# Kernel optimization log

Hardware: AMD Instinct MI355X
Metric: run time of the kernel (lower is better)

## Reference

```python
import jax, jax.numpy as jnp
import numpy as np

B, T, C, H = 8, 2048, 1024, 64

def setup_inputs() -> dict:
    key = jax.random.key(0)
    k1, k2, k3, k4 = jax.random.split(key, 4)
    x = jax.random.normal(k1, (B, T, C), dtype=jnp.float32)
    # torch nn.Linear default init ~ U(-1/sqrt(in), 1/sqrt(in)); scale kept small for stability
    s = 1.0 / np.sqrt(C)
    Wq = jax.random.uniform(k2, (C, H), dtype=jnp.float32, minval=-s, maxval=s)
    Wk = jax.random.uniform(k3, (C, H), dtype=jnp.float32, minval=-s, maxval=s)
    Wv = jax.random.uniform(k4, (C, H), dtype=jnp.float32, minval=-s, maxval=s)
    return {"x": x, "Wq": Wq, "Wk": Wk, "Wv": Wv}

def reference(x, Wq, Wk, Wv):
    # x: [B,T,C]; Wq/Wk/Wv: [C,H] (equivalent to torch Linear weight transposed)
    Q = jnp.einsum('btc,ch->bth', x, Wq)
    K = jnp.einsum('btc,ch->bth', x, Wk)
    V = jnp.einsum('btc,ch->bth', x, Wv)
    H_ = Q.shape[-1]
    scale = 1.0 / jnp.sqrt(jnp.asarray(H_, dtype=Q.dtype))
    w = jnp.einsum('bqh,bkh->bqk', Q, K) * scale  # [B,T,T]
    T_ = x.shape[1]
    causal = jnp.tril(jnp.ones((T_, T_), dtype=bool))
    w = jnp.where(causal, w, -jnp.inf)
    w = jax.nn.softmax(w, axis=-1)
    out = jnp.einsum('bqk,bkh->bqh', w, V)  # [B,T,H]
    return out
```

## Files before the change

### kernel.cpp

```cpp
#include <hip/hip_runtime.h>
#include <math.h>

#define Bb 8
#define Tt 2048
#define Cc 1024
#define Hh 64
#define BT (Bb * Tt)
#define SLOG2E 0.18033688011112042f

typedef __attribute__((ext_vector_type(8))) short short8;
typedef __attribute__((ext_vector_type(4))) float floatx4;

__device__ inline unsigned short f2bf(float f) {
  unsigned int u = __builtin_bit_cast(unsigned int, f);
  u += 0x7fff + ((u >> 16) & 1);
  return (unsigned short)(u >> 16);
}
__device__ inline float bf2f(unsigned short u) {
  unsigned int x = ((unsigned int)u) << 16;
  return __builtin_bit_cast(float, x);
}

__global__ __launch_bounds__(256) void wconv2(
    const float* __restrict__ Wq, const float* __restrict__ Wk,
    const float* __restrict__ Wv, unsigned short* __restrict__ WTf) {
  int bid = blockIdx.x;
  int w = bid >> 5;
  int kc = bid & 31;
  const float* __restrict__ W = (w == 0) ? Wq : (w == 1 ? Wk : Wv);
  int t = threadIdx.x;
  int hg = t >> 6, quad = (t >> 4) & 3, lrow = t & 15;
  int g = w * 4 + hg;
  int h = hg * 16 + lrow;
  unsigned short tmp[8];
#pragma unroll
  for (int j = 0; j < 8; ++j)
    tmp[j] = f2bf(W[(size_t)(kc * 32 + quad * 8 + j) * Hh + h]);
  unsigned short* dst = &WTf[((size_t)(g * 32 + kc) * 64 + quad * 16 + lrow) * 8];
  *(ushort4*)dst = make_ushort4(tmp[0], tmp[1], tmp[2], tmp[3]);
  *(ushort4*)(dst + 4) = make_ushort4(tmp[4], tmp[5], tmp[6], tmp[7]);
}

__global__ __launch_bounds__(256) void qkv5(
    const float* __restrict__ x, const unsigned short* __restrict__ WTf,
    unsigned short* __restrict__ Qb, unsigned short* __restrict__ Kb,
    unsigned short* __restrict__ VTt) {
  __shared__ __align__(16) unsigned short Af[2048];

  int mt = blockIdx.x;
  int t = threadIdx.x;
  int wv = t >> 6, lane = t & 63;
  int lrow = lane & 15, quad = lane >> 4;

  floatx4 acc[2][3];
#pragma unroll
  for (int g2 = 0; g2 < 2; ++g2)
#pragma unroll
    for (int j = 0; j < 3; ++j)
#pragma unroll
      for (int r = 0; r < 4; ++r) acc[g2][j][r] = 0.f;

  int srow = t >> 3, scg = t & 7;
  int skc2 = scg >> 2, squad = scg & 3;
  int sslot = ((srow >> 4) * 2 + skc2) * 64 + squad * 16 +
              (((srow & 15) + squad + 4 * skc2) & 15);
  const float* xp = x + (size_t)(mt * 32 + srow) * Cc + scg * 8;

  int aslot[2][2];
#pragma unroll
  for (int g2 = 0; g2 < 2; ++g2)
#pragma unroll
    for (int kc2 = 0; kc2 < 2; ++kc2)
      aslot[g2][kc2] = ((g2 * 2 + kc2) * 64 + quad * 16 +
                        ((lrow + quad + 4 * kc2) & 15)) * 8;

  const unsigned short* wbase[3];
#pragma unroll
  for (int j = 0; j < 3; ++j)
    wbase[j] = WTf + (size_t)(wv * 3 + j) * 32 * 512 + lane * 8;

  float4 nv0 = *(const float4*)xp;
  float4 nv1 = *(const float4*)(xp + 4);

  for (int kk = 0; kk < 16; ++kk) {
    __syncthreads();
    short8 a;
    a[0] = (short)f2bf(nv0.x); a[1] = (short)f2bf(nv0.y);
    a[2] = (short)f2bf(nv0.z); a[3] = (short)f2bf(nv0.w);
    a[4] = (short)f2bf(nv1.x); a[5] = (short)f2bf(nv1.y);
    a[6] = (short)f2bf(nv1.z); a[7] = (short)f2bf(nv1.w);
    *(short8*)&Af[sslot * 8] = a;
    if (kk < 15) {
      nv0 = *(const float4*)(xp + (kk + 1) * 64);
      nv1 = *(const float4*)(xp + (kk + 1) * 64 + 4);
    }
    __syncthreads();

    short8 bf[3][2];
    int kg = kk * 2;
#pragma unroll
    for (int j = 0; j < 3; ++j)
#pragma unroll
      for (int kc2 = 0; kc2 < 2; ++kc2)
        bf[j][kc2] = *(const short8*)(wbase[j] + (size_t)(kg + kc2) * 512);
    short8 af[2][2];
#pragma unroll
    for (int g2 = 0; g2 < 2; ++g2)
#pragma unroll
      for (int kc2 = 0; kc2 < 2; ++kc2)
        af[g2][kc2] = *(const short8*)&Af[aslot[g2][kc2]];
#pragma unroll
    for (int g2 = 0; g2 < 2; ++g2)
#pragma unroll
      for (int j = 0; j < 3; ++j) {
        acc[g2][j] = __builtin_amdgcn_mfma_f32_16x16x32_bf16(af[g2][0], bf[j][0], acc[g2][j], 0, 0, 0);
        acc[g2][j] = __builtin_amdgcn_mfma_f32_16x16x32_bf16(af[g2][1], bf[j][1], acc[g2][j], 0, 0, 0);
      }
  }

#pragma unroll
  for (int g2 = 0; g2 < 2; ++g2) {
    int tok0 = mt * 32 + g2 * 16 + quad * 4;
#pragma unroll
    for (int j = 0; j < 3; ++j) {
      int nbase = (wv * 3 + j) * 16;
      if (nbase >= 128) {
        int h = nbase - 128 + lrow;
        *(ushort4*)&VTt[(size_t)(tok0 >> 6) * 4096 + h * 64 + (tok0 & 63)] =
            make_ushort4(f2bf(acc[g2][j][0]), f2bf(acc[g2][j][1]),
                         f2bf(acc[g2][j][2]), f2bf(acc[g2][j][3]));
      } else {
        unsigned short* dst = (nbase >= 64) ? Kb : Qb;
        int col = (nbase & 63) + lrow;
#pragma unroll
        for (int r = 0; r < 4; ++r)
          dst[(size_t)(tok0 + r) * Hh + col] = f2bf(acc[g2][j][r]);
      }
    }
  }
}

__global__ __launch_bounds__(512) void attn3(
    const unsigned short* __restrict__ Qb, const unsigned short* __restrict__ Kb,
    const unsigned short* __restrict__ VTt, float* __restrict__ out) {
  __shared__ __align__(16) unsigned char smem[33 * 1024];
  unsigned short* Pall = (unsigned short*)smem;
  unsigned short* Ocomb = (unsigned short*)smem;
  float* Lcomb = (float*)(smem + 32768);

  int bid = blockIdx.x;
  int b = bid >> 5;
  int j = bid & 31;
  int t = threadIdx.x;
  int wv = t >> 6, lane = t & 63;
  int lrow = lane & 15, quad = lane >> 4;

  unsigned short* Pw = Pall + wv * 2048;

  short8 ones;
#pragma unroll
  for (int i = 0; i < 8; ++i) ones[i] = (short)0x3F80;

  for (int half = 0; half < 2; ++half) {
    int qt = half ? (63 - j) : j;
    int q0 = qt * 32;
    int nkt = (qt >> 1) + 1;

    short8 aq[2][2];
#pragma unroll
    for (int qs = 0; qs < 2; ++qs)
#pragma unroll
      for (int kc = 0; kc < 2; ++kc)
        aq[qs][kc] = *(const short8*)
            &Qb[(size_t)(b * Tt + q0 + qs * 16 + lrow) * Hh + kc * 32 + quad * 8];

    floatx4 acc_o[2][4];
    floatx4 acc_l[2];
#pragma unroll
    for (int qs = 0; qs < 2; ++qs) {
#pragma unroll
      for (int r = 0; r < 4; ++r) acc_l[qs][r] = 0.f;
#pragma unroll
      for (int hs = 0; hs < 4; ++hs)
#pragma unroll
        for (int r = 0; r < 4; ++r) acc_o[qs][hs][r] = 0.f;
    }

    for (int kt = wv; kt < nkt; kt += 8) {
      int kbase = b * Tt + kt * 64;
      short8 kf[4][2], vf[4][2];
#pragma unroll
      for (int sn = 0; sn < 4; ++sn)
#pragma unroll
        for (int kc = 0; kc < 2; ++kc)
          kf[sn][kc] = *(const short8*)
              &Kb[(size_t)(kbase + sn * 16 + lrow) * Hh + kc * 32 + quad * 8];
      int ktile = b * 32 + kt;
#pragma unroll
      for (int hs = 0; hs < 4; ++hs)
#pragma unroll
        for (int kc = 0; kc < 2; ++kc)
          vf[hs][kc] = *(const short8*)
              &VTt[(size_t)ktile * 4096 + (hs * 16 + lrow) * 64 + kc * 32 + quad * 8];

      floatx4 s[2][4];
#pragma unroll
      for (int qs = 0; qs < 2; ++qs)
#pragma unroll
        for (int sn = 0; sn < 4; ++sn) {
          floatx4 z;
#pragma unroll
          for (int r = 0; r < 4; ++r) z[r] = 0.f;
          z = __builtin_amdgcn_mfma_f32_16x16x32_bf16(aq[qs][0], kf[sn][0], z, 0, 0, 0);
          z = __builtin_amdgcn_mfma_f32_16x16x32_bf16(aq[qs][1], kf[sn][1], z, 0, 0, 0);
          s[qs][sn] = z;
        }

      bool diag = (kt == nkt - 1);
#pragma unroll
      for (int qs = 0; qs < 2; ++qs)
#pragma unroll
        for (int sn = 0; sn < 4; ++sn) {
          int k5 = (sn & 1) * 16 + lrow;
          int slot = qs * 2 + (sn >> 1);
          int rlbase = (k5 >> 3) * 16;
#pragma unroll
          for (int r = 0; r < 4; ++r) {
            float v = s[qs][sn][r] * SLOG2E;
            if (diag) {
              int gk = kt * 64 + sn * 16 + lrow;
              int gq = q0 + qs * 16 + quad * 4 + r;
              if (gk > gq) v = -INFINITY;
            }
            float p = exp2f(v);
            Pw[slot * 512 + (rlbase + quad * 4 + r) * 8 + (k5 & 7)] = f2bf(p);
          }
        }

      short8 ap[2][2];
#pragma unroll
      for (int qs = 0; qs < 2; ++qs)
#pragma unroll
        for (int kc = 0; kc < 2; ++kc)
          ap[qs][kc] = *(const short8*)&Pw[(qs * 2 + kc) * 512 + lane * 8];

#pragma unroll
      for (int qs = 0; qs < 2; ++qs) {
        acc_l[qs] = __builtin_amdgcn_mfma_f32_16x16x32_bf16(ap[qs][0], ones, acc_l[qs], 0, 0, 0);
        acc_l[qs] = __builtin_amdgcn_mfma_f32_16x16x32_bf16(ap[qs][1], ones, acc_l[qs], 0, 0, 0);
#pragma unroll
        for (int hs = 0; hs < 4; ++hs) {
          acc_o[qs][hs] = __builtin_amdgcn_mfma_f32_16x16x32_bf16(ap[qs][0], vf[hs][0], acc_o[qs][hs], 0, 0, 0);
          acc_o[qs][hs] = __builtin_amdgcn_mfma_f32_16x16x32_bf16(ap[qs][1], vf[hs][1], acc_o[qs][hs], 0, 0, 0);
        }
      }
    }

#pragma unroll
    for (int qs = 0; qs < 2; ++qs)
#pragma unroll
      for (int hs = 0; hs < 4; ++hs) {
        int s8 = qs * 4 + hs;
        *(ushort4*)&Ocomb[((wv * 8 + s8) * 64 + lane) * 4] =
            make_ushort4(f2bf(acc_o[qs][hs][0]), f2bf(acc_o[qs][hs][1]),
                         f2bf(acc_o[qs][hs][2]), f2bf(acc_o[qs][hs][3]));
      }
    if (lrow == 0) {
#pragma unroll
      for (int qs = 0; qs < 2; ++qs)
#pragma unroll
        for (int r = 0; r < 4; ++r)
          Lcomb[wv * 32 + qs * 16 + quad * 4 + r] = acc_l[qs][r];
    }
    __syncthreads();

    {
      int qsub = wv >> 2, hs = wv & 3;
      float o[4] = {0.f, 0.f, 0.f, 0.f};
#pragma unroll
      for (int w = 0; w < 8; ++w) {
        ushort4 pk = *(const ushort4*)&Ocomb[((w * 8 + wv) * 64 + lane) * 4];
        o[0] += bf2f(pk.x); o[1] += bf2f(pk.y);
        o[2] += bf2f(pk.z); o[3] += bf2f(pk.w);
      }
#pragma unroll
      for (int r = 0; r < 4; ++r) {
        float lv = 0.f;
#pragma unroll
        for (int w = 0; w < 8; ++w)
          lv += Lcomb[w * 32 + qsub * 16 + quad * 4 + r];
        int row = q0 + qsub * 16 + quad * 4 + r;
        out[(size_t)(b * Tt + row) * Hh + hs * 16 + lrow] = o[r] / lv;
      }
    }
    __syncthreads();
  }
}

extern "C" void kernel_launch(void* const* d_in, const int* in_sizes, int n_in,
                              void* d_out, int out_size, void* d_ws, size_t ws_size,
                              hipStream_t stream) {
  const float* x = (const float*)d_in[0];
  const float* Wq = (const float*)d_in[1];
  const float* Wk = (const float*)d_in[2];
  const float* Wv = (const float*)d_in[3];
  float* out = (float*)d_out;

  unsigned short* WTf = (unsigned short*)d_ws;
  unsigned short* Qb = WTf + 192 * 1024;
  unsigned short* Kb = Qb + (size_t)BT * Hh;
  unsigned short* VTt = Kb + (size_t)BT * Hh;

  wconv2<<<dim3(96), dim3(256), 0, stream>>>(Wq, Wk, Wv, WTf);
  qkv5<<<dim3(512), dim3(256), 0, stream>>>(x, WTf, Qb, Kb, VTt);
  attn3<<<dim3(256), dim3(512), 0, stream>>>(Qb, Kb, VTt, out);
}
```

Baseline: 131.8 us.

## Schedule attention tiles dynamically via atomic counter and double-buffer QKV LDS

The attention kernel drops the fixed pairing of two query tiles per block. Blocks now use 4 waves and pull (batch, query-tile) work items from a global atomic counter, longest tiles first, so the causal triangle is balanced across CUs. The counter is reset inside the projection kernel, which relies on stream ordering between the two kernels. The projection kernel also double-buffers its LDS A tile, which removes one barrier per k-step and overlaps the global loads of x with the MFMAs. Fewer waves per attention tile means less key parallelism inside each block, and every work item now costs an extra atomic and barrier.

```diff
diff --git a/kernel.cpp b/kernel.cpp
--- a/kernel.cpp
+++ b/kernel.cpp
@@ -41,11 +41,13 @@
   *(ushort4*)(dst + 4) = make_ushort4(tmp[4], tmp[5], tmp[6], tmp[7]);
 }
 
-__global__ __launch_bounds__(256) void qkv5(
+__global__ __launch_bounds__(256) void qkv6(
     const float* __restrict__ x, const unsigned short* __restrict__ WTf,
     unsigned short* __restrict__ Qb, unsigned short* __restrict__ Kb,
-    unsigned short* __restrict__ VTt) {
-  __shared__ __align__(16) unsigned short Af[2048];
+    unsigned short* __restrict__ VTt, int* __restrict__ cnt) {
+  __shared__ __align__(16) unsigned short Af[2][2048];
+
+  if (blockIdx.x == 0 && threadIdx.x == 0) *cnt = 0;
 
   int mt = blockIdx.x;
   int t = threadIdx.x;
@@ -79,23 +81,25 @@
   for (int j = 0; j < 3; ++j)
     wbase[j] = WTf + (size_t)(wv * 3 + j) * 32 * 512 + lane * 8;
 
-  float4 nv0 = *(const float4*)xp;
-  float4 nv1 = *(const float4*)(xp + 4);
+  {
+    float4 v0 = *(const float4*)xp;
+    float4 v1 = *(const float4*)(xp + 4);
+    short8 a;
+    a[0] = (short)f2bf(v0.x); a[1] = (short)f2bf(v0.y);
+    a[2] = (short)f2bf(v0.z); a[3] = (short)f2bf(v0.w);
+    a[4] = (short)f2bf(v1.x); a[5] = (short)f2bf(v1.y);
+    a[6] = (short)f2bf(v1.z); a[7] = (short)f2bf(v1.w);
+    *(short8*)&Af[0][sslot * 8] = a;
+  }
+  __syncthreads();
 
   for (int kk = 0; kk < 16; ++kk) {
-    __syncthreads();
-    short8 a;
-    a[0] = (short)f2bf(nv0.x); a[1] = (short)f2bf(nv0.y);
-    a[2] = (short)f2bf(nv0.z); a[3] = (short)f2bf(nv0.w);
-    a[4] = (short)f2bf(nv1.x); a[5] = (short)f2bf(nv1.y);
-    a[6] = (short)f2bf(nv1.z); a[7] = (short)f2bf(nv1.w);
-    *(short8*)&Af[sslot * 8] = a;
+    int cur = kk & 1;
+    float4 v0, v1;
     if (kk < 15) {
-      nv0 = *(const float4*)(xp + (kk + 1) * 64);
-      nv1 = *(const float4*)(xp + (kk + 1) * 64 + 4);
-    }
-    __syncthreads();
-
+      v0 = *(const float4*)(xp + (kk + 1) * 64);
+      v1 = *(const float4*)(xp + (kk + 1) * 64 + 4);
+    }
     short8 bf[3][2];
     int kg = kk * 2;
 #pragma unroll
@@ -108,7 +112,7 @@
     for (int g2 = 0; g2 < 2; ++g2)
 #pragma unroll
       for (int kc2 = 0; kc2 < 2; ++kc2)
-        af[g2][kc2] = *(const short8*)&Af[aslot[g2][kc2]];
+        af[g2][kc2] = *(const short8*)&Af[cur][aslot[g2][kc2]];
 #pragma unroll
     for (int g2 = 0; g2 < 2; ++g2)
 #pragma unroll
@@ -116,6 +120,15 @@
         acc[g2][j] = __builtin_amdgcn_mfma_f32_16x16x32_bf16(af[g2][0], bf[j][0], acc[g2][j], 0, 0, 0);
         acc[g2][j] = __builtin_amdgcn_mfma_f32_16x16x32_bf16(af[g2][1], bf[j][1], acc[g2][j], 0, 0, 0);
       }
+    if (kk < 15) {
+      short8 a;
+      a[0] = (short)f2bf(v0.x); a[1] = (short)f2bf(v0.y);
+      a[2] = (short)f2bf(v0.z); a[3] = (short)f2bf(v0.w);
+      a[4] = (short)f2bf(v1.x); a[5] = (short)f2bf(v1.y);
+      a[6] = (short)f2bf(v1.z); a[7] = (short)f2bf(v1.w);
+      *(short8*)&Af[1 - cur][sslot * 8] = a;
+      __syncthreads();
+    }
   }
 
 #pragma unroll
@@ -140,29 +153,32 @@
   }
 }
 
-__global__ __launch_bounds__(512) void attn3(
+__global__ __launch_bounds__(256) void attn5(
     const unsigned short* __restrict__ Qb, const unsigned short* __restrict__ Kb,
-    const unsigned short* __restrict__ VTt, float* __restrict__ out) {
-  __shared__ __align__(16) unsigned char smem[33 * 1024];
+    const unsigned short* __restrict__ VTt, float* __restrict__ out,
+    int* __restrict__ cnt) {
+  __shared__ __align__(16) unsigned char smem[16384 + 512];
+  __shared__ int sU;
   unsigned short* Pall = (unsigned short*)smem;
   unsigned short* Ocomb = (unsigned short*)smem;
-  float* Lcomb = (float*)(smem + 32768);
-
-  int bid = blockIdx.x;
-  int b = bid >> 5;
-  int j = bid & 31;
+  float* Lcomb = (float*)(smem + 16384);
+
   int t = threadIdx.x;
   int wv = t >> 6, lane = t & 63;
   int lrow = lane & 15, quad = lane >> 4;
-
   unsigned short* Pw = Pall + wv * 2048;
 
   short8 ones;
 #pragma unroll
   for (int i = 0; i < 8; ++i) ones[i] = (short)0x3F80;
 
-  for (int half = 0; half < 2; ++half) {
-    int qt = half ? (63 - j) : j;
+  for (;;) {
+    if (t == 0) sU = atomicAdd(cnt, 1);
+    __syncthreads();
+    int u = sU;
+    if (u >= 512) break;
+    int qt = 63 - (u >> 3);
+    int b = u & 7;
     int q0 = qt * 32;
     int nkt = (qt >> 1) + 1;
 
@@ -186,7 +202,7 @@
         for (int r = 0; r < 4; ++r) acc_o[qs][hs][r] = 0.f;
     }
 
-    for (int kt = wv; kt < nkt; kt += 8) {
+    for (int kt = wv; kt < nkt; kt += 4) {
       int kbase = b * Tt + kt * 64;
       short8 kf[4][2], vf[4][2];
 #pragma unroll
@@ -274,12 +290,14 @@
     }
     __syncthreads();
 
-    {
-      int qsub = wv >> 2, hs = wv & 3;
+#pragma unroll
+    for (int s2 = 0; s2 < 2; ++s2) {
+      int slot = wv * 2 + s2;
+      int qsub = slot >> 2, hs = slot & 3;
       float o[4] = {0.f, 0.f, 0.f, 0.f};
 #pragma unroll
-      for (int w = 0; w < 8; ++w) {
-        ushort4 pk = *(const ushort4*)&Ocomb[((w * 8 + wv) * 64 + lane) * 4];
+      for (int w = 0; w < 4; ++w) {
+        ushort4 pk = *(const ushort4*)&Ocomb[((w * 8 + slot) * 64 + lane) * 4];
         o[0] += bf2f(pk.x); o[1] += bf2f(pk.y);
         o[2] += bf2f(pk.z); o[3] += bf2f(pk.w);
       }
@@ -287,13 +305,12 @@
       for (int r = 0; r < 4; ++r) {
         float lv = 0.f;
 #pragma unroll
-        for (int w = 0; w < 8; ++w)
+        for (int w = 0; w < 4; ++w)
           lv += Lcomb[w * 32 + qsub * 16 + quad * 4 + r];
         int row = q0 + qsub * 16 + quad * 4 + r;
         out[(size_t)(b * Tt + row) * Hh + hs * 16 + lrow] = o[r] / lv;
       }
     }
-    __syncthreads();
   }
 }
 
@@ -310,8 +327,9 @@
   unsigned short* Qb = WTf + 192 * 1024;
   unsigned short* Kb = Qb + (size_t)BT * Hh;
   unsigned short* VTt = Kb + (size_t)BT * Hh;
+  int* cnt = (int*)(VTt + (size_t)BT * Hh);
 
   wconv2<<<dim3(96), dim3(256), 0, stream>>>(Wq, Wk, Wv, WTf);
-  qkv5<<<dim3(512), dim3(256), 0, stream>>>(x, WTf, Qb, Kb, VTt);
-  attn3<<<dim3(256), dim3(512), 0, stream>>>(Qb, Kb, VTt, out);
-}
+  qkv6<<<dim3(512), dim3(256), 0, stream>>>(x, WTf, Qb, Kb, VTt, cnt);
+  attn5<<<dim3(1024), dim3(256), 0, stream>>>(Qb, Kb, VTt, out, cnt);
+}
```

Result: slower. 146.5 us (+11.2%).

## Store Q/K/V in MFMA fragment order and double-buffer x tiles in projection

Applied to the files above, without the earlier changes.

The projection kernel now writes Q, K and V in a pre-swizzled MFMA-fragment layout, staged through shared memory so each lane issues contiguous 16-byte global stores. The attention kernel can then load operands as fully contiguous per-lane vectors instead of strided row gathers. The projection loop also double-buffers the converted x tile in LDS, cutting one barrier per iteration. The cost is more shared memory and an extra LDS transpose pass in the epilogue.

```diff
diff --git a/kernel.cpp b/kernel.cpp
--- a/kernel.cpp
+++ b/kernel.cpp
@@ -20,6 +20,7 @@
   unsigned int x = ((unsigned int)u) << 16;
   return __builtin_bit_cast(float, x);
 }
+
 
 __global__ __launch_bounds__(256) void wconv2(
     const float* __restrict__ Wq, const float* __restrict__ Wk,
@@ -41,11 +42,11 @@
   *(ushort4*)(dst + 4) = make_ushort4(tmp[4], tmp[5], tmp[6], tmp[7]);
 }
 
-__global__ __launch_bounds__(256) void qkv5(
+__global__ __launch_bounds__(256) void qkv7(
     const float* __restrict__ x, const unsigned short* __restrict__ WTf,
-    unsigned short* __restrict__ Qb, unsigned short* __restrict__ Kb,
-    unsigned short* __restrict__ VTt) {
-  __shared__ __align__(16) unsigned short Af[2048];
+    unsigned short* __restrict__ Qf, unsigned short* __restrict__ Kf,
+    unsigned short* __restrict__ Vf) {
+  __shared__ __align__(16) unsigned short smem7[6656];
 
   int mt = blockIdx.x;
   int t = threadIdx.x;
@@ -79,23 +80,25 @@
   for (int j = 0; j < 3; ++j)
     wbase[j] = WTf + (size_t)(wv * 3 + j) * 32 * 512 + lane * 8;
 
-  float4 nv0 = *(const float4*)xp;
-  float4 nv1 = *(const float4*)(xp + 4);
+  {
+    float4 v0 = *(const float4*)xp;
+    float4 v1 = *(const float4*)(xp + 4);
+    short8 a;
+    a[0] = (short)f2bf(v0.x); a[1] = (short)f2bf(v0.y);
+    a[2] = (short)f2bf(v0.z); a[3] = (short)f2bf(v0.w);
+    a[4] = (short)f2bf(v1.x); a[5] = (short)f2bf(v1.y);
+    a[6] = (short)f2bf(v1.z); a[7] = (short)f2bf(v1.w);
+    *(short8*)&smem7[sslot * 8] = a;
+  }
+  __syncthreads();
 
   for (int kk = 0; kk < 16; ++kk) {
-    __syncthreads();
-    short8 a;
-    a[0] = (short)f2bf(nv0.x); a[1] = (short)f2bf(nv0.y);
-    a[2] = (short)f2bf(nv0.z); a[3] = (short)f2bf(nv0.w);
-    a[4] = (short)f2bf(nv1.x); a[5] = (short)f2bf(nv1.y);
-    a[6] = (short)f2bf(nv1.z); a[7] = (short)f2bf(nv1.w);
-    *(short8*)&Af[sslot * 8] = a;
+    int cur = kk & 1;
+    float4 v0, v1;
     if (kk < 15) {
-      nv0 = *(const float4*)(xp + (kk + 1) * 64);
-      nv1 = *(const float4*)(xp + (kk + 1) * 64 + 4);
-    }
-    __syncthreads();
-
+      v0 = *(const float4*)(xp + (kk + 1) * 64);
+      v1 = *(const float4*)(xp + (kk + 1) * 64 + 4);
+    }
     short8 bf[3][2];
     int kg = kk * 2;
 #pragma unroll
@@ -108,7 +111,7 @@
     for (int g2 = 0; g2 < 2; ++g2)
 #pragma unroll
       for (int kc2 = 0; kc2 < 2; ++kc2)
-        af[g2][kc2] = *(const short8*)&Af[aslot[g2][kc2]];
+        af[g2][kc2] = *(const short8*)&smem7[cur * 2048 + aslot[g2][kc2]];
 #pragma unroll
     for (int g2 = 0; g2 < 2; ++g2)
 #pragma unroll
@@ -116,33 +119,59 @@
         acc[g2][j] = __builtin_amdgcn_mfma_f32_16x16x32_bf16(af[g2][0], bf[j][0], acc[g2][j], 0, 0, 0);
         acc[g2][j] = __builtin_amdgcn_mfma_f32_16x16x32_bf16(af[g2][1], bf[j][1], acc[g2][j], 0, 0, 0);
       }
+    if (kk < 15) {
+      short8 a;
+      a[0] = (short)f2bf(v0.x); a[1] = (short)f2bf(v0.y);
+      a[2] = (short)f2bf(v0.z); a[3] = (short)f2bf(v0.w);
+      a[4] = (short)f2bf(v1.x); a[5] = (short)f2bf(v1.y);
+      a[6] = (short)f2bf(v1.z); a[7] = (short)f2bf(v1.w);
+      *(short8*)&smem7[(1 - cur) * 2048 + sslot * 8] = a;
+      __syncthreads();
+    }
   }
 
-#pragma unroll
-  for (int g2 = 0; g2 < 2; ++g2) {
-    int tok0 = mt * 32 + g2 * 16 + quad * 4;
+  __syncthreads();
+#pragma unroll
+  for (int g2 = 0; g2 < 2; ++g2)
 #pragma unroll
     for (int j = 0; j < 3; ++j) {
-      int nbase = (wv * 3 + j) * 16;
-      if (nbase >= 128) {
-        int h = nbase - 128 + lrow;
-        *(ushort4*)&VTt[(size_t)(tok0 >> 6) * 4096 + h * 64 + (tok0 & 63)] =
-            make_ushort4(f2bf(acc[g2][j][0]), f2bf(acc[g2][j][1]),
-                         f2bf(acc[g2][j][2]), f2bf(acc[g2][j][3]));
-      } else {
-        unsigned short* dst = (nbase >= 64) ? Kb : Qb;
-        int col = (nbase & 63) + lrow;
-#pragma unroll
-        for (int r = 0; r < 4; ++r)
-          dst[(size_t)(tok0 + r) * Hh + col] = f2bf(acc[g2][j][r]);
-      }
+      int col = (wv * 3 + j) * 16 + lrow;
+#pragma unroll
+      for (int r = 0; r < 4; ++r)
+        smem7[(g2 * 16 + quad * 4 + r) * 208 + col] = f2bf(acc[g2][j][r]);
+    }
+  __syncthreads();
+#pragma unroll
+  for (int fi = 0; fi < 3; ++fi) {
+    int idx = fi * 256 + t;
+    if (idx < 512) {
+      int which = idx >> 8;
+      int sub = idx & 255;
+      int g2k = sub >> 6, lane_s = sub & 63;
+      int g2_ = g2k >> 1, kc_ = g2k & 1;
+      int tokrow = g2_ * 16 + (lane_s & 15);
+      int hbase = which * 64 + kc_ * 32 + (lane_s >> 4) * 8;
+      short8 v = *(const short8*)&smem7[tokrow * 208 + hbase];
+      unsigned short* dstf = which ? Kf : Qf;
+      *(short8*)&dstf[((size_t)(mt * 2 + g2_) * 2 + kc_) * 512 + lane_s * 8] = v;
+    } else {
+      int sub = idx - 512;
+      int hs = sub >> 6, lane_s = sub & 63;
+      int hcol = 128 + hs * 16 + (lane_s & 15);
+      int tok0 = (lane_s >> 4) * 8;
+      unsigned short tmp[8];
+#pragma unroll
+      for (int jj = 0; jj < 8; ++jj) tmp[jj] = smem7[(tok0 + jj) * 208 + hcol];
+      unsigned short* dv = &Vf[((size_t)(mt * 4 + hs)) * 512 + lane_s * 8];
+      *(ushort4*)dv = make_ushort4(tmp[0], tmp[1], tmp[2], tmp[3]);
+      *(ushort4*)(dv + 4) = make_ushort4(tmp[4], tmp[5], tmp[6], tmp[7]);
     }
   }
 }
 
-__global__ __launch_bounds__(512) void attn3(
-    const unsigned short* __restrict__ Qb, const unsigned short* __restrict__ Kb,
-    const unsigned short* __restrict__ VTt, float* __restrict__ out) {
+__global__ __launch_bounds__(512) void attn6(
+    const unsigned short* __restrict__ Qf, const unsigned short* __restrict__ Kf,
+    const unsigned short* __restrict__ Vf, float* __restrict__ out) {
   __shared__ __align__(16) unsigned char smem[33 * 1024];
   unsigned short* Pall = (unsigned short*)smem;
   unsigned short* Ocomb = (unsigned short*)smem;
@@ -165,6 +194,7 @@
     int qt = half ? (63 - j) : j;
     int q0 = qt * 32;
     int nkt = (qt >> 1) + 1;
+    int qtile16 = b * 128 + qt * 2;
 
     short8 aq[2][2];
 #pragma unroll
@@ -172,7 +202,7 @@
 #pragma unroll
       for (int kc = 0; kc < 2; ++kc)
         aq[qs][kc] = *(const short8*)
-            &Qb[(size_t)(b * Tt + q0 + qs * 16 + lrow) * Hh + kc * 32 + quad * 8];
+            &Qf[((size_t)(qtile16 + qs) * 2 + kc) * 512 + lane * 8];
 
     floatx4 acc_o[2][4];
     floatx4 acc_l[2];
@@ -187,21 +217,21 @@
     }
 
     for (int kt = wv; kt < nkt; kt += 8) {
-      int kbase = b * Tt + kt * 64;
+      int ktile16 = b * 128 + kt * 4;
+      int ktile32 = b * 64 + kt * 2;
       short8 kf[4][2], vf[4][2];
 #pragma unroll
       for (int sn = 0; sn < 4; ++sn)
 #pragma unroll
         for (int kc = 0; kc < 2; ++kc)
           kf[sn][kc] = *(const short8*)
-              &Kb[(size_t)(kbase + sn * 16 + lrow) * Hh + kc * 32 + quad * 8];
-      int ktile = b * 32 + kt;
+              &Kf[((size_t)(ktile16 + sn) * 2 + kc) * 512 + lane * 8];
 #pragma unroll
       for (int hs = 0; hs < 4; ++hs)
 #pragma unroll
         for (int kc = 0; kc < 2; ++kc)
           vf[hs][kc] = *(const short8*)
-              &VTt[(size_t)ktile * 4096 + (hs * 16 + lrow) * 64 + kc * 32 + quad * 8];
+              &Vf[((size_t)(ktile32 + kc) * 4 + hs) * 512 + lane * 8];
 
       floatx4 s[2][4];
 #pragma unroll
@@ -307,11 +337,11 @@
   float* out = (float*)d_out;
 
   unsigned short* WTf = (unsigned short*)d_ws;
-  unsigned short* Qb = WTf + 192 * 1024;
-  unsigned short* Kb = Qb + (size_t)BT * Hh;
-  unsigned short* VTt = Kb + (size_t)BT * Hh;
+  unsigned short* Qf = WTf + 192 * 1024;
+  unsigned short* Kf = Qf + (size_t)(BT / 16) * 2 * 512;
+  unsigned short* Vf = Kf + (size_t)(BT / 16) * 2 * 512;
 
   wconv2<<<dim3(96), dim3(256), 0, stream>>>(Wq, Wk, Wv, WTf);
-  qkv5<<<dim3(512), dim3(256), 0, stream>>>(x, WTf, Qb, Kb, VTt);
-  attn3<<<dim3(256), dim3(512), 0, stream>>>(Qb, Kb, VTt, out);
-}
+  qkv7<<<dim3(512), dim3(256), 0, stream>>>(x, WTf, Qf, Kf, Vf);
+  attn6<<<dim3(256), dim3(512), 0, stream>>>(Qf, Kf, Vf, out);
+}
```

Result: no change. 132.4 us (+0.5%).
